# Optimization experiments

Measured on AMD Instinct MI355X. Metric: run time of the kernel, lower is better.

Reference implementation:

```python
import jax, jax.numpy as jnp
import numpy as np

N_RECTS = 200000
GRID = 256


def setup_inputs() -> dict:
    key = jax.random.key(0)
    k1, k2, k3 = jax.random.split(key, 3)
    # unit placement region [0,1] x [0,1]
    boundary = jnp.array([[0.0, 0.0], [1.0, 1.0]], dtype=jnp.float32)
    # lower-left corners in [0, 1); cell sizes ~ a few bins wide (bin = 1/GRID)
    xy = jax.random.uniform(k1, (N_RECTS, 2), dtype=jnp.float32)
    dims = jax.random.uniform(k2, (N_RECTS, 2), dtype=jnp.float32) * (3.0 / GRID)
    charge_weight = jax.random.uniform(k3, (N_RECTS,), dtype=jnp.float32) + 0.5
    return {"boundary": boundary, "xy": xy, "dims": dims,
            "charge_weight": charge_weight, "grid_size": GRID}


def reference(boundary, xy, dims, charge_weight, grid_size):
    G = grid_size
    dtype = xy.dtype
    xmin, ymin = boundary[0, 0], boundary[0, 1]
    xmax, ymax = boundary[1, 0], boundary[1, 1]
    lx = (xmax - xmin) / G
    ly = (ymax - ymin) / G
    idx = jnp.arange(G, dtype=dtype)
    gx0 = xmin + idx * lx   # [G] bin left edges
    gy0 = ymin + idx * ly
    gx1 = gx0 + lx
    gy1 = gy0 + ly
    bx0 = xy[:, 0]
    by0 = xy[:, 1]
    bx1 = bx0 + dims[:, 0]
    by1 = by0 + dims[:, 1]
    # per-rect / per-bin 1D overlaps: [N, G]
    ox = jnp.maximum(jnp.minimum(gx1[None, :], bx1[:, None]) -
                     jnp.maximum(gx0[None, :], bx0[:, None]), 0.0)
    oy = jnp.maximum(jnp.minimum(gy1[None, :], by1[:, None]) -
                     jnp.maximum(gy0[None, :], by0[:, None]), 0.0)
    # sum over chunks of weighted outer products == one big matmul:
    # field[i, j] = sum_n w[n] * ox[n, i] * oy[n, j]
    field = jnp.einsum('ni,nj->ij', ox * charge_weight[:, None], oy)
    return field / (lx * ly)
```

## Files before the change

kernel.cpp:

```cpp
#include <hip/hip_runtime.h>
#include <math.h>

__global__ __launch_bounds__(1024)
void strip_scan(const float* __restrict__ boundary,
                const float2* __restrict__ xy,
                const float2* __restrict__ dims,
                const float* __restrict__ w,
                float* __restrict__ ws,
                int G, int R, int rows, int n_rects)
{
    extern __shared__ float acc[];
    const int b   = blockIdx.x;
    const int s   = b / R;
    const int r   = b % R;
    const int tid = threadIdx.x;
    const int stripElems = rows * G;
    const int row0 = s * rows;
    const int row1 = row0 + rows - 1;

    for (int c = tid; c < stripElems; c += blockDim.x) acc[c] = 0.0f;
    __syncthreads();

    const float xmin = boundary[0], ymin = boundary[1];
    const float xmax = boundary[2], ymax = boundary[3];
    const float lx = (xmax - xmin) / (float)G;
    const float ly = (ymax - ymin) / (float)G;
    const float inv_lx = (float)G / (xmax - xmin);
    const float inv_ly = (float)G / (ymax - ymin);
    const float inv_area = inv_lx * inv_ly;

    const int chunk = (n_rects + R - 1) / R;
    const int lo = r * chunk;
    const int hi = min(lo + chunk, n_rects);

    for (int n = lo + tid; n < hi; n += blockDim.x) {
        float2 p = xy[n];
        float2 d = dims[n];
        const float bx0 = p.x, bx1 = p.x + d.x;

        int ri0 = (int)floorf((bx0 - xmin) * inv_lx);
        int ri1 = (int)floorf((bx1 - xmin) * inv_lx);
        int i0 = max(max(ri0, 0), row0);
        int i1 = min(min(ri1, G - 1), row1);
        if (i0 > i1) continue;

        const float by0 = p.y, by1 = p.y + d.y;
        int j0 = max((int)floorf((by0 - ymin) * inv_ly), 0);
        int j1 = min((int)floorf((by1 - ymin) * inv_ly), G - 1);
        if (j0 > j1) continue;

        const float cw = w[n] * inv_area;

        if (i1 - i0 <= 3 && j1 - j0 <= 3) {
            float oxv[4], oyv[4];
            #pragma unroll
            for (int di = 0; di < 4; ++di) {
                int   i   = i0 + di;
                float gx0 = xmin + (float)i * lx;
                float ox  = fminf(gx0 + lx, bx1) - fmaxf(gx0, bx0);
                oxv[di] = (i <= i1) ? fmaxf(ox, 0.0f) : 0.0f;
            }
            #pragma unroll
            for (int dj = 0; dj < 4; ++dj) {
                int   j   = j0 + dj;
                float gy0 = ymin + (float)j * ly;
                float oy  = fminf(gy0 + ly, by1) - fmaxf(gy0, by0);
                oyv[dj] = (j <= j1) ? fmaxf(oy, 0.0f) : 0.0f;
            }
            #pragma unroll
            for (int di = 0; di < 4; ++di) {
                if (oxv[di] > 0.0f) {
                    float  cox  = cw * oxv[di];
                    float* rowp = acc + (i0 + di - row0) * G + j0;
                    #pragma unroll
                    for (int dj = 0; dj < 4; ++dj) {
                        if (oyv[dj] > 0.0f)
                            atomicAdd(rowp + dj, cox * oyv[dj]);
                    }
                }
            }
        } else {
            for (int i = i0; i <= i1; ++i) {
                float gx0 = xmin + (float)i * lx;
                float ox  = fmaxf(fminf(gx0 + lx, bx1) - fmaxf(gx0, bx0), 0.0f);
                if (ox <= 0.0f) continue;
                float cox = cw * ox;
                float* rowp = acc + (i - row0) * G;
                for (int j = j0; j <= j1; ++j) {
                    float gy0 = ymin + (float)j * ly;
                    float oy  = fminf(gy0 + ly, by1) - fmaxf(gy0, by0);
                    if (oy > 0.0f) atomicAdd(rowp + j, cox * oy);
                }
            }
        }
    }
    __syncthreads();

    float4* dst = (float4*)(ws + (size_t)b * stripElems);
    const float4* src = (const float4*)acc;
    const int nvec = stripElems >> 2;
    for (int c = tid; c < nvec; c += blockDim.x) dst[c] = src[c];
}

__global__ __launch_bounds__(256)
void reduce_strips(const float* __restrict__ ws,
                   float* __restrict__ out,
                   int G, int R, int rows)
{
    const int c = blockIdx.x * blockDim.x + threadIdx.x;
    if (c >= G * G) return;
    const int i = c / G;
    const int j = c - i * G;
    const int s = i / rows;
    const int stripElems = rows * G;
    const int local = (i - s * rows) * G + j;

    const float* base = ws + (size_t)s * R * stripElems + local;
    float sum = 0.0f;
    #pragma unroll 16
    for (int r = 0; r < R; ++r)
        sum += base[(size_t)r * stripElems];
    out[c] = sum;
}

__global__ void scatter_direct(const float* __restrict__ boundary,
                               const float2* __restrict__ xy,
                               const float2* __restrict__ dims,
                               const float* __restrict__ w,
                               float* __restrict__ out,
                               int G, int n_rects)
{
    int n = blockIdx.x * blockDim.x + threadIdx.x;
    if (n >= n_rects) return;
    float xmin = boundary[0], ymin = boundary[1];
    float xmax = boundary[2], ymax = boundary[3];
    float lx = (xmax - xmin) / (float)G;
    float ly = (ymax - ymin) / (float)G;
    float2 p = xy[n]; float2 d = dims[n];
    float bx0 = p.x, by0 = p.y, bx1 = bx0 + d.x, by1 = by0 + d.y;
    float cw = w[n] / (lx * ly);
    int i0 = max((int)floorf((bx0 - xmin) / lx), 0);
    int i1 = min((int)floorf((bx1 - xmin) / lx), G - 1);
    int j0 = max((int)floorf((by0 - ymin) / ly), 0);
    int j1 = min((int)floorf((by1 - ymin) / ly), G - 1);
    for (int i = i0; i <= i1; ++i) {
        float gx0 = xmin + (float)i * lx;
        float ox = fmaxf(fminf(gx0 + lx, bx1) - fmaxf(gx0, bx0), 0.0f);
        if (ox <= 0.0f) continue;
        float cox = cw * ox;
        for (int j = j0; j <= j1; ++j) {
            float gy0 = ymin + (float)j * ly;
            float oy = fmaxf(fminf(gy0 + ly, by1) - fmaxf(gy0, by0), 0.0f);
            if (oy > 0.0f) atomicAdd(out + (size_t)i * G + j, cox * oy);
        }
    }
}

extern "C" void kernel_launch(void* const* d_in, const int* in_sizes, int n_in,
                              void* d_out, int out_size, void* d_ws, size_t ws_size,
                              hipStream_t stream) {
    const float*  boundary = (const float*)d_in[0];
    const float2* xy       = (const float2*)d_in[1];
    const float2* dims     = (const float2*)d_in[2];
    const float*  cweight  = (const float*)d_in[3];
    float* out = (float*)d_out;
    const int n_rects = in_sizes[1] / 2;

    int G = (int)lround(sqrt((double)out_size));
    const bool square = ((long long)G * G == (long long)out_size) && G > 0;

    int S = 0, rows = 0;
    if (square) {
        for (int cand = 1; cand <= 256; cand <<= 1) {
            if (G % cand) continue;
            long long bytes = (long long)(G / cand) * G * 4;
            if (bytes <= 64 * 1024) { S = cand; rows = G / cand; break; }
        }
    }
    int R = 0;
    if (S > 0) {
        R = 256 / S;
        if (R < 1) R = 1;
        long long need = (long long)S * R * rows * G * 4;
        while (R > 1 && need > (long long)ws_size) {
            R >>= 1;
            need = (long long)S * R * rows * G * 4;
        }
        if (need > (long long)ws_size) R = 0;
    }

    if (R > 0) {
        float* ws = (float*)d_ws;
        const int stripBytes = rows * G * 4;
        strip_scan<<<S * R, 1024, stripBytes, stream>>>(
            boundary, xy, dims, cweight, ws, G, R, rows, n_rects);
        reduce_strips<<<(G * G + 255) / 256, 256, 0, stream>>>(
            ws, out, G, R, rows);
    } else {
        hipMemsetAsync(out, 0, (size_t)out_size * sizeof(float), stream);
        const int block = 256;
        scatter_direct<<<(n_rects + block - 1) / block, block, 0, stream>>>(
            boundary, xy, dims, cweight, out, G, n_rects);
    }
}
```

Baseline: 82.41 us.

## Fuse strip scan and reduction into one cooperative kernel with grid sync

Adds a cooperative kernel that builds per-block shared-memory strips, writes them to workspace, does a grid-wide sync, then reduces the partial strips in the same launch. This removes the second kernel launch and its launch gap. The per-strip replica count drops from 256/S to at most 16, so each block scans more rectangles but there are fewer partials to reduce. The old two-kernel path stays as a fallback if the cooperative launch fails, and its fallback kernel's 4x4 unrolled fast path is removed.

```diff
diff --git a/kernel.cpp b/kernel.cpp
--- a/kernel.cpp
+++ b/kernel.cpp
@@ -1,5 +1,127 @@
 #include <hip/hip_runtime.h>
+#include <hip/hip_cooperative_groups.h>
 #include <math.h>
+
+namespace cg = cooperative_groups;
+
+__global__ __launch_bounds__(1024)
+void fused_field(const float* __restrict__ boundary,
+                 const float2* __restrict__ xy,
+                 const float2* __restrict__ dims,
+                 const float* __restrict__ w,
+                 float* __restrict__ ws,
+                 float* __restrict__ out,
+                 int G, int R, int rows, int n_rects)
+{
+    extern __shared__ float acc[];
+    const int b   = blockIdx.x;
+    const int s   = b / R;
+    const int r   = b % R;
+    const int tid = threadIdx.x;
+    const int stripElems = rows * G;
+    const int row0 = s * rows;
+    const int row1 = row0 + rows - 1;
+
+    for (int c = tid; c < stripElems; c += blockDim.x) acc[c] = 0.0f;
+    __syncthreads();
+
+    const float xmin = boundary[0], ymin = boundary[1];
+    const float xmax = boundary[2], ymax = boundary[3];
+    const float lx = (xmax - xmin) / (float)G;
+    const float ly = (ymax - ymin) / (float)G;
+    const float inv_lx = (float)G / (xmax - xmin);
+    const float inv_ly = (float)G / (ymax - ymin);
+    const float inv_area = inv_lx * inv_ly;
+
+    const int chunk = (n_rects + R - 1) / R;
+    const int lo = r * chunk;
+    const int hi = min(lo + chunk, n_rects);
+
+    for (int n = lo + tid; n < hi; n += blockDim.x) {
+        float2 p = xy[n];
+        float2 d = dims[n];
+        const float bx0 = p.x, bx1 = p.x + d.x;
+
+        int ri0 = (int)floorf((bx0 - xmin) * inv_lx);
+        int ri1 = (int)floorf((bx1 - xmin) * inv_lx);
+        int i0 = max(max(ri0, 0), row0);
+        int i1 = min(min(ri1, G - 1), row1);
+        if (i0 > i1) continue;
+
+        const float by0 = p.y, by1 = p.y + d.y;
+        int j0 = max((int)floorf((by0 - ymin) * inv_ly), 0);
+        int j1 = min((int)floorf((by1 - ymin) * inv_ly), G - 1);
+        if (j0 > j1) continue;
+
+        const float cw = w[n] * inv_area;
+
+        if (i1 - i0 <= 3 && j1 - j0 <= 3) {
+            float oxv[4], oyv[4];
+            #pragma unroll
+            for (int di = 0; di < 4; ++di) {
+                int   i   = i0 + di;
+                float gx0 = xmin + (float)i * lx;
+                float ox  = fminf(gx0 + lx, bx1) - fmaxf(gx0, bx0);
+                oxv[di] = (i <= i1) ? fmaxf(ox, 0.0f) : 0.0f;
+            }
+            #pragma unroll
+            for (int dj = 0; dj < 4; ++dj) {
+                int   j   = j0 + dj;
+                float gy0 = ymin + (float)j * ly;
+                float oy  = fminf(gy0 + ly, by1) - fmaxf(gy0, by0);
+                oyv[dj] = (j <= j1) ? fmaxf(oy, 0.0f) : 0.0f;
+            }
+            #pragma unroll
+            for (int di = 0; di < 4; ++di) {
+                if (oxv[di] > 0.0f) {
+                    float  cox  = cw * oxv[di];
+                    float* rowp = acc + (i0 + di - row0) * G + j0;
+                    #pragma unroll
+                    for (int dj = 0; dj < 4; ++dj) {
+                        if (oyv[dj] > 0.0f)
+                            atomicAdd(rowp + dj, cox * oyv[dj]);
+                    }
+                }
+            }
+        } else {
+            for (int i = i0; i <= i1; ++i) {
+                float gx0 = xmin + (float)i * lx;
+                float ox  = fmaxf(fminf(gx0 + lx, bx1) - fmaxf(gx0, bx0), 0.0f);
+                if (ox <= 0.0f) continue;
+                float cox = cw * ox;
+                float* rowp = acc + (i - row0) * G;
+                for (int j = j0; j <= j1; ++j) {
+                    float gy0 = ymin + (float)j * ly;
+                    float oy  = fminf(gy0 + ly, by1) - fmaxf(gy0, by0);
+                    if (oy > 0.0f) atomicAdd(rowp + j, cox * oy);
+                }
+            }
+        }
+    }
+    __syncthreads();
+
+    {
+        float4* dst = (float4*)(ws + (size_t)b * stripElems);
+        const float4* src = (const float4*)acc;
+        const int nvec = stripElems >> 2;
+        for (int c = tid; c < nvec; c += blockDim.x) dst[c] = src[c];
+    }
+
+    __threadfence();
+    cg::this_grid().sync();
+
+    const int per = (stripElems + R - 1) / R;
+    const int c0  = r * per;
+    const int c1  = min(c0 + per, stripElems);
+    const float* base = ws + (size_t)s * R * stripElems;
+    for (int c = c0 + tid; c < c1; c += blockDim.x) {
+        float sum = 0.0f;
+        #pragma unroll 8
+        for (int rr = 0; rr < R; ++rr)
+            sum += base[(size_t)rr * stripElems + c];
+        out[(size_t)s * stripElems + c] = sum;
+    }
+}
 
 __global__ __launch_bounds__(1024)
 void strip_scan(const float* __restrict__ boundary,
@@ -37,65 +159,28 @@
         float2 p = xy[n];
         float2 d = dims[n];
         const float bx0 = p.x, bx1 = p.x + d.x;
-
-        int ri0 = (int)floorf((bx0 - xmin) * inv_lx);
-        int ri1 = (int)floorf((bx1 - xmin) * inv_lx);
-        int i0 = max(max(ri0, 0), row0);
-        int i1 = min(min(ri1, G - 1), row1);
+        int i0 = max(max((int)floorf((bx0 - xmin) * inv_lx), 0), row0);
+        int i1 = min(min((int)floorf((bx1 - xmin) * inv_lx), G - 1), row1);
         if (i0 > i1) continue;
-
         const float by0 = p.y, by1 = p.y + d.y;
         int j0 = max((int)floorf((by0 - ymin) * inv_ly), 0);
         int j1 = min((int)floorf((by1 - ymin) * inv_ly), G - 1);
         if (j0 > j1) continue;
-
         const float cw = w[n] * inv_area;
-
-        if (i1 - i0 <= 3 && j1 - j0 <= 3) {
-            float oxv[4], oyv[4];
-            #pragma unroll
-            for (int di = 0; di < 4; ++di) {
-                int   i   = i0 + di;
-                float gx0 = xmin + (float)i * lx;
-                float ox  = fminf(gx0 + lx, bx1) - fmaxf(gx0, bx0);
-                oxv[di] = (i <= i1) ? fmaxf(ox, 0.0f) : 0.0f;
-            }
-            #pragma unroll
-            for (int dj = 0; dj < 4; ++dj) {
-                int   j   = j0 + dj;
+        for (int i = i0; i <= i1; ++i) {
+            float gx0 = xmin + (float)i * lx;
+            float ox  = fmaxf(fminf(gx0 + lx, bx1) - fmaxf(gx0, bx0), 0.0f);
+            if (ox <= 0.0f) continue;
+            float cox = cw * ox;
+            float* rowp = acc + (i - row0) * G;
+            for (int j = j0; j <= j1; ++j) {
                 float gy0 = ymin + (float)j * ly;
                 float oy  = fminf(gy0 + ly, by1) - fmaxf(gy0, by0);
-                oyv[dj] = (j <= j1) ? fmaxf(oy, 0.0f) : 0.0f;
-            }
-            #pragma unroll
-            for (int di = 0; di < 4; ++di) {
-                if (oxv[di] > 0.0f) {
-                    float  cox  = cw * oxv[di];
-                    float* rowp = acc + (i0 + di - row0) * G + j0;
-                    #pragma unroll
-                    for (int dj = 0; dj < 4; ++dj) {
-                        if (oyv[dj] > 0.0f)
-                            atomicAdd(rowp + dj, cox * oyv[dj]);
-                    }
-                }
-            }
-        } else {
-            for (int i = i0; i <= i1; ++i) {
-                float gx0 = xmin + (float)i * lx;
-                float ox  = fmaxf(fminf(gx0 + lx, bx1) - fmaxf(gx0, bx0), 0.0f);
-                if (ox <= 0.0f) continue;
-                float cox = cw * ox;
-                float* rowp = acc + (i - row0) * G;
-                for (int j = j0; j <= j1; ++j) {
-                    float gy0 = ymin + (float)j * ly;
-                    float oy  = fminf(gy0 + ly, by1) - fmaxf(gy0, by0);
-                    if (oy > 0.0f) atomicAdd(rowp + j, cox * oy);
-                }
+                if (oy > 0.0f) atomicAdd(rowp + j, cox * oy);
             }
         }
     }
     __syncthreads();
-
     float4* dst = (float4*)(ws + (size_t)b * stripElems);
     const float4* src = (const float4*)acc;
     const int nvec = stripElems >> 2;
@@ -114,7 +199,6 @@
     const int s = i / rows;
     const int stripElems = rows * G;
     const int local = (i - s * rows) * G + j;
-
     const float* base = ws + (size_t)s * R * stripElems + local;
     float sum = 0.0f;
     #pragma unroll 16
@@ -164,7 +248,7 @@
     const float2* dims     = (const float2*)d_in[2];
     const float*  cweight  = (const float*)d_in[3];
     float* out = (float*)d_out;
-    const int n_rects = in_sizes[1] / 2;
+    int n_rects = in_sizes[1] / 2;
 
     int G = (int)lround(sqrt((double)out_size));
     const bool square = ((long long)G * G == (long long)out_size) && G > 0;
@@ -177,6 +261,30 @@
             if (bytes <= 64 * 1024) { S = cand; rows = G / cand; break; }
         }
     }
+
+    int Rf = 0;
+    if (S > 0) {
+        Rf = 16;
+        while (Rf > 1 && (S * Rf > 256 ||
+               (long long)Rf * G * G * 4 > (long long)ws_size)) Rf >>= 1;
+        if (S * Rf > 256 || (long long)Rf * G * G * 4 > (long long)ws_size) Rf = 0;
+    }
+
+    if (Rf > 0) {
+        float* ws = (float*)d_ws;
+        int stripBytes = rows * G * 4;
+        void* args[] = {
+            (void*)&boundary, (void*)&xy, (void*)&dims, (void*)&cweight,
+            (void*)&ws, (void*)&out, (void*)&G, (void*)&Rf, (void*)&rows,
+            (void*)&n_rects
+        };
+        hipError_t err = hipLaunchCooperativeKernel(
+            (const void*)fused_field, dim3(S * Rf), dim3(1024),
+            args, stripBytes, stream);
+        if (err == hipSuccess) return;
+        (void)hipGetLastError();
+    }
+
     int R = 0;
     if (S > 0) {
         R = 256 / S;
```

Result: slower. 152.8 us (+85.4%).
